# Optimization experiments

Measured on AMD Instinct MI355X. Metric: run time of the kernel, lower is better.

Reference implementation:

```python
import jax, jax.numpy as jnp
import numpy as np


def setup_inputs() -> dict:
    key = jax.random.key(0)
    k1, k2, k3, k4 = jax.random.split(key, 4)
    E = 1_600_000
    N = 100_000
    IN, OUT = 128, 256
    edge_index = jax.random.randint(k1, (2, E), 0, N, dtype=jnp.int32)
    time_encoding = jax.random.normal(k2, (E, IN), dtype=jnp.float32)
    # Linear(in_channels, out_channels): weight [OUT, IN], bias [OUT]
    bound = 1.0 / np.sqrt(IN)
    W = jax.random.uniform(k3, (OUT, IN), minval=-bound, maxval=bound, dtype=jnp.float32)
    b = jax.random.uniform(k4, (OUT,), minval=-bound, maxval=bound, dtype=jnp.float32)
    return {"edge_index": edge_index, "time_encoding": time_encoding,
            "num_nodes": N, "W": W, "b": b}


def reference(edge_index, time_encoding, num_nodes, W, b):
    # scatter-add per-edge time encodings into destination-node buckets
    col = edge_index[1]
    agg = jax.ops.segment_sum(time_encoding, col, num_segments=num_nodes)  # [N, IN]
    # dense projection: Linear -> x @ W.T + b
    return agg @ W.T + b  # [N, OUT]
```

## Files before the change

kernel.cpp:

```cpp
#include <hip/hip_runtime.h>
#include <hip/hip_bf16.h>

#define IN_CH 128
#define OUT_CH 256
#define BLK_SCAN 1024
#define AGG_STRIDE 132

typedef __bf16 bf16x8 __attribute__((ext_vector_type(8)));
typedef float f32x4 __attribute__((ext_vector_type(4)));

__device__ inline unsigned short f2bf(float f) {
  union { float f; unsigned int u; } v; v.f = f;
  unsigned int u = v.u;
  u += 0x7FFFu + ((u >> 16) & 1u);
  return (unsigned short)(u >> 16);
}

__device__ inline float bfhi2f(unsigned int u) {
  union { unsigned int u; float f; } v; v.u = u & 0xFFFF0000u; return v.f;
}
__device__ inline float bflo2f(unsigned int u) {
  union { unsigned int u; float f; } v; v.u = u << 16; return v.f;
}

__global__ void initB_kernel(const float* __restrict__ W, unsigned short* __restrict__ Bpack,
                             int* __restrict__ cnt, int nzero) {
  int i = blockIdx.x * blockDim.x + threadIdx.x;
  if (i < nzero) cnt[i] = 0;
  if (i < IN_CH * OUT_CH) {
    const int j  = i & 7;
    const int c  = (i >> 3) & 15;
    const int kb = (i >> 7) & 3;
    const int ks = (i >> 9) & 3;
    const int tn = i >> 11;
    Bpack[i] = f2bf(W[(size_t)(tn * 16 + c) * IN_CH + ks * 32 + kb * 8 + j]);
  }
}

__global__ void hist_kernel(const int* __restrict__ col, int E, int* __restrict__ count) {
  int i = blockIdx.x * blockDim.x + threadIdx.x;
  int b = i * 4;
  if (b + 4 <= E) {
    const int4 c = *(const int4*)(col + b);
    atomicAdd(&count[c.x], 1);
    atomicAdd(&count[c.y], 1);
    atomicAdd(&count[c.z], 1);
    atomicAdd(&count[c.w], 1);
  } else {
    for (int j = b; j < E; ++j) atomicAdd(&count[col[j]], 1);
  }
}

__global__ __launch_bounds__(BLK_SCAN) void scan_block_kernel(
    const int* __restrict__ count, int N, int* __restrict__ excl, int* __restrict__ bsum) {
  __shared__ int wsum[16];
  const int tid = threadIdx.x;
  const int i = blockIdx.x * BLK_SCAN + tid;
  const int v = (i < N) ? count[i] : 0;
  int x = v;
#pragma unroll
  for (int d = 1; d < 64; d <<= 1) {
    int t = __shfl_up(x, d, 64);
    if ((tid & 63) >= d) x += t;
  }
  if ((tid & 63) == 63) wsum[tid >> 6] = x;
  __syncthreads();
  if (tid < 16) {
    int s = wsum[tid];
#pragma unroll
    for (int d = 1; d < 16; d <<= 1) {
      int t = __shfl_up(s, d, 16);
      if (tid >= d) s += t;
    }
    wsum[tid] = s;
  }
  __syncthreads();
  const int w = tid >> 6;
  const int prefix = (w == 0) ? 0 : wsum[w - 1];
  if (i < N) excl[i] = prefix + x - v;
  if (tid == BLK_SCAN - 1) bsum[blockIdx.x] = prefix + x;
}

__global__ void scan_bsum_kernel(int* __restrict__ bsum, int nb) {
  __shared__ int tmp[256];
  const int tid = threadIdx.x;
  int run = 0;
  for (int s = 0; s < nb; s += 256) {
    int v = (s + tid < nb) ? bsum[s + tid] : 0;
    tmp[tid] = v;
    __syncthreads();
    for (int d = 1; d < 256; d <<= 1) {
      int t = (tid >= d) ? tmp[tid - d] : 0;
      __syncthreads();
      tmp[tid] += t;
      __syncthreads();
    }
    if (s + tid < nb) bsum[s + tid] = run + tmp[tid] - v;
    run += tmp[255];
    __syncthreads();
  }
}

__global__ void add_offsets_kernel(int* __restrict__ excl, const int* __restrict__ bsum,
                                   int* __restrict__ cursor, int N) {
  int i = blockIdx.x * blockDim.x + threadIdx.x;
  if (i < N) {
    int o = excl[i] + bsum[i / BLK_SCAN];
    excl[i] = o;
    cursor[i] = o;
  }
}

__global__ __launch_bounds__(256) void bin_kernel(
    const float* __restrict__ te, const int* __restrict__ col,
    int* __restrict__ cursor, unsigned int* __restrict__ binned, int E) {
  const int lane = threadIdx.x & 63;
  const int gw = (blockIdx.x * 256 + threadIdx.x) >> 6;
  const int nw = (gridDim.x * 256) >> 6;
  for (int base = gw * 8; base < E; base += nw * 8) {
    int ne = E - base; if (ne > 8) ne = 8;
    int mypos = 0;
    if (lane < ne) {
      mypos = atomicAdd(&cursor[col[base + lane]], 1);
    }
#pragma unroll
    for (int j = 0; j < 8; ++j) {
      if (j < ne) {
        const int pos = __builtin_amdgcn_readlane(mypos, j);
        const float2 v = *(const float2*)(te + (size_t)(base + j) * IN_CH + lane * 2);
        binned[(size_t)pos * 64 + lane] =
            (unsigned int)f2bf(v.x) | ((unsigned int)f2bf(v.y) << 16);
      }
    }
  }
}

__global__ __launch_bounds__(256) void phase2_kernel(
    const unsigned int* __restrict__ binned, const int* __restrict__ start,
    const int* __restrict__ cend, const unsigned short* __restrict__ Bpack,
    const float* __restrict__ bias, float* __restrict__ out, int N) {
  __shared__ float agg[16][AGG_STRIDE];
  const int tid = threadIdx.x;
  const int wave = tid >> 6;
  const int lane = tid & 63;
  const int half = lane >> 5;
  const int li   = lane & 31;
  const int m0 = blockIdx.x * 16;

  int s0[4], e0[4];
  float acc[4][4];
  uint2 v[4][8];
#pragma unroll
  for (int q = 0; q < 4; ++q) {
    const int n = m0 + wave * 4 + q;
    s0[q] = (n < N) ? start[n] : 0;
    e0[q] = (n < N) ? cend[n] : 0;
#pragma unroll
    for (int c = 0; c < 4; ++c) acc[q][c] = 0.f;
  }
#pragma unroll
  for (int q = 0; q < 4; ++q) {
#pragma unroll
    for (int j = 0; j < 8; ++j) {
      int row = s0[q] + 2 * j + half;
      row = (row < e0[q]) ? row : (e0[q] > s0[q] ? e0[q] - 1 : 0);
      v[q][j] = *(const uint2*)(binned + (size_t)row * 64 + li * 2);
    }
  }
#pragma unroll
  for (int q = 0; q < 4; ++q) {
    const int rem = e0[q] - s0[q];
#pragma unroll
    for (int j = 0; j < 8; ++j) {
      const float c = (2 * j + half < rem) ? 1.f : 0.f;
      acc[q][0] = fmaf(c, bflo2f(v[q][j].x), acc[q][0]);
      acc[q][1] = fmaf(c, bfhi2f(v[q][j].x), acc[q][1]);
      acc[q][2] = fmaf(c, bflo2f(v[q][j].y), acc[q][2]);
      acc[q][3] = fmaf(c, bfhi2f(v[q][j].y), acc[q][3]);
    }
    for (int r0 = s0[q] + 16; r0 < e0[q]; r0 += 16) {
      const int rem2 = e0[q] - r0;
      uint2 w[8];
#pragma unroll
      for (int j = 0; j < 8; ++j) {
        int row = r0 + 2 * j + half;
        row = (row < e0[q]) ? row : (e0[q] - 1);
        w[j] = *(const uint2*)(binned + (size_t)row * 64 + li * 2);
      }
#pragma unroll
      for (int j = 0; j < 8; ++j) {
        const float c = (2 * j + half < rem2) ? 1.f : 0.f;
        acc[q][0] = fmaf(c, bflo2f(w[j].x), acc[q][0]);
        acc[q][1] = fmaf(c, bfhi2f(w[j].x), acc[q][1]);
        acc[q][2] = fmaf(c, bflo2f(w[j].y), acc[q][2]);
        acc[q][3] = fmaf(c, bfhi2f(w[j].y), acc[q][3]);
      }
    }
    acc[q][0] += __shfl_down(acc[q][0], 32);
    acc[q][1] += __shfl_down(acc[q][1], 32);
    acc[q][2] += __shfl_down(acc[q][2], 32);
    acc[q][3] += __shfl_down(acc[q][3], 32);
    if (half == 0) {
      *(float4*)(&agg[wave * 4 + q][4 * li]) =
          make_float4(acc[q][0], acc[q][1], acc[q][2], acc[q][3]);
    }
  }
  __syncthreads();

  const int r  = lane & 15;
  const int kb = lane >> 4;

  bf16x8 a[4];
#pragma unroll
  for (int ks = 0; ks < 4; ++ks) {
    bf16x8 t;
#pragma unroll
    for (int j = 0; j < 8; ++j) t[j] = (__bf16)agg[r][ks * 32 + kb * 8 + j];
    a[ks] = t;
  }

  f32x4 accm[4];
#pragma unroll
  for (int ct = 0; ct < 4; ++ct) accm[ct] = (f32x4){0.f, 0.f, 0.f, 0.f};

#pragma unroll
  for (int ct = 0; ct < 4; ++ct) {
    const int tn = wave * 4 + ct;
#pragma unroll
    for (int ks = 0; ks < 4; ++ks) {
      const bf16x8 bb = *(const bf16x8*)(Bpack + (size_t)((((tn * 4 + ks) * 4 + kb) * 16 + r) * 8));
      accm[ct] = __builtin_amdgcn_mfma_f32_16x16x32_bf16(a[ks], bb, accm[ct], 0, 0, 0);
    }
  }

#pragma unroll
  for (int ct = 0; ct < 4; ++ct) {
    const int colo = wave * 64 + ct * 16 + r;
    const float bv = bias[colo];
#pragma unroll
    for (int j = 0; j < 4; ++j) {
      const int m = m0 + kb * 4 + j;
      if (m < N) out[(size_t)m * OUT_CH + colo] = accm[ct][j] + bv;
    }
  }
}

extern "C" void kernel_launch(void* const* d_in, const int* in_sizes, int n_in,
                              void* d_out, int out_size, void* d_ws, size_t ws_size,
                              hipStream_t stream) {
  const int* edge_index = (const int*)d_in[0];
  const float* te       = (const float*)d_in[1];
  const float* W        = (const float*)d_in[3];
  const float* bias     = (const float*)d_in[4];
  float* out            = (float*)d_out;

  const int E = in_sizes[0] / 2;
  const int N = out_size / OUT_CH;
  const int* col = edge_index + E;

  const int Np = (N + 3) & ~3;

  char* p = (char*)d_ws;
  unsigned short* Bpack = (unsigned short*)p;      p += 65536;
  int* cnt    = (int*)p;                           p += (size_t)Np * 4;
  int* start  = (int*)p;                           p += (size_t)Np * 4;
  int* cursor = (int*)p;                           p += (size_t)Np * 4;
  int* bsum   = (int*)p;                           p += 4096 * 4;
  p = (char*)(((uintptr_t)p + 255) & ~(uintptr_t)255);
  unsigned int* binned = (unsigned int*)p;

  const int nb = (N + BLK_SCAN - 1) / BLK_SCAN;
  const int init_n = (N > IN_CH * OUT_CH) ? N : IN_CH * OUT_CH;
  const int K = (N + 15) / 16;

  hipLaunchKernelGGL(initB_kernel, dim3((init_n + 255) / 256), dim3(256), 0, stream,
                     W, Bpack, cnt, N);
  hipLaunchKernelGGL(hist_kernel, dim3((E / 4 + 255) / 256), dim3(256), 0, stream,
                     col, E, cnt);
  hipLaunchKernelGGL(scan_block_kernel, dim3(nb), dim3(BLK_SCAN), 0, stream,
                     cnt, N, start, bsum);
  hipLaunchKernelGGL(scan_bsum_kernel, dim3(1), dim3(256), 0, stream, bsum, nb);
  hipLaunchKernelGGL(add_offsets_kernel, dim3((N + 255) / 256), dim3(256), 0, stream,
                     start, bsum, cursor, N);
  hipLaunchKernelGGL(bin_kernel, dim3(2048), dim3(256), 0, stream,
                     te, col, cursor, binned, E);
  hipLaunchKernelGGL(phase2_kernel, dim3(K), dim3(256), 0, stream,
                     binned, start, cursor, Bpack, bias, out, N);
}
```

Before: 453.6 us.

## Split edge binning and aggregation into two chunks with bf16 partial sums

Edges are split into two halves. Each half gets its own histogram and cursor range. The first half is binned and aggregated into a bf16 per-node partial buffer. The second half is then binned and aggregated, and adds the partials before the MFMA projection. The intent is to shrink the binned data in flight between the bin and aggregate passes so more of it stays in the last-level cache instead of going out to HBM. The te loads and output stores also become nontemporal. The cost is two extra kernel launches, an extra write and read of the per-node partial buffer, and an extra bf16 rounding of the partial sums.

```diff
diff --git a/kernel.cpp b/kernel.cpp
--- a/kernel.cpp
+++ b/kernel.cpp
@@ -8,6 +8,7 @@
 
 typedef __bf16 bf16x8 __attribute__((ext_vector_type(8)));
 typedef float f32x4 __attribute__((ext_vector_type(4)));
+typedef float f32x2 __attribute__((ext_vector_type(2)));
 
 __device__ inline unsigned short f2bf(float f) {
   union { float f; unsigned int u; } v; v.f = f;
@@ -15,7 +16,6 @@
   u += 0x7FFFu + ((u >> 16) & 1u);
   return (unsigned short)(u >> 16);
 }
-
 __device__ inline float bfhi2f(unsigned int u) {
   union { unsigned int u; float f; } v; v.u = u & 0xFFFF0000u; return v.f;
 }
@@ -37,26 +37,27 @@
   }
 }
 
-__global__ void hist_kernel(const int* __restrict__ col, int E, int* __restrict__ count) {
+__global__ void hist2_kernel(const int* __restrict__ col, int E, int E2,
+                             int* __restrict__ cnt2, int N) {
   int i = blockIdx.x * blockDim.x + threadIdx.x;
   int b = i * 4;
   if (b + 4 <= E) {
     const int4 c = *(const int4*)(col + b);
-    atomicAdd(&count[c.x], 1);
-    atomicAdd(&count[c.y], 1);
-    atomicAdd(&count[c.z], 1);
-    atomicAdd(&count[c.w], 1);
+    atomicAdd(&cnt2[((b + 0) >= E2 ? N : 0) + c.x], 1);
+    atomicAdd(&cnt2[((b + 1) >= E2 ? N : 0) + c.y], 1);
+    atomicAdd(&cnt2[((b + 2) >= E2 ? N : 0) + c.z], 1);
+    atomicAdd(&cnt2[((b + 3) >= E2 ? N : 0) + c.w], 1);
   } else {
-    for (int j = b; j < E; ++j) atomicAdd(&count[col[j]], 1);
+    for (int j = b; j < E; ++j) atomicAdd(&cnt2[(j >= E2 ? N : 0) + col[j]], 1);
   }
 }
 
 __global__ __launch_bounds__(BLK_SCAN) void scan_block_kernel(
-    const int* __restrict__ count, int N, int* __restrict__ excl, int* __restrict__ bsum) {
+    const int* __restrict__ count, int NN, int* __restrict__ excl, int* __restrict__ bsum) {
   __shared__ int wsum[16];
   const int tid = threadIdx.x;
   const int i = blockIdx.x * BLK_SCAN + tid;
-  const int v = (i < N) ? count[i] : 0;
+  const int v = (i < NN) ? count[i] : 0;
   int x = v;
 #pragma unroll
   for (int d = 1; d < 64; d <<= 1) {
@@ -77,7 +78,7 @@
   __syncthreads();
   const int w = tid >> 6;
   const int prefix = (w == 0) ? 0 : wsum[w - 1];
-  if (i < N) excl[i] = prefix + x - v;
+  if (i < NN) excl[i] = prefix + x - v;
   if (tid == BLK_SCAN - 1) bsum[blockIdx.x] = prefix + x;
 }
 
@@ -102,9 +103,9 @@
 }
 
 __global__ void add_offsets_kernel(int* __restrict__ excl, const int* __restrict__ bsum,
-                                   int* __restrict__ cursor, int N) {
+                                   int* __restrict__ cursor, int NN) {
   int i = blockIdx.x * blockDim.x + threadIdx.x;
-  if (i < N) {
+  if (i < NN) {
     int o = excl[i] + bsum[i / BLK_SCAN];
     excl[i] = o;
     cursor[i] = o;
@@ -113,12 +114,12 @@
 
 __global__ __launch_bounds__(256) void bin_kernel(
     const float* __restrict__ te, const int* __restrict__ col,
-    int* __restrict__ cursor, unsigned int* __restrict__ binned, int E) {
+    int* __restrict__ cursor, unsigned int* __restrict__ binned, int lo, int hi) {
   const int lane = threadIdx.x & 63;
   const int gw = (blockIdx.x * 256 + threadIdx.x) >> 6;
   const int nw = (gridDim.x * 256) >> 6;
-  for (int base = gw * 8; base < E; base += nw * 8) {
-    int ne = E - base; if (ne > 8) ne = 8;
+  for (int base = lo + gw * 8; base < hi; base += nw * 8) {
+    int ne = hi - base; if (ne > 8) ne = 8;
     int mypos = 0;
     if (lane < ne) {
       mypos = atomicAdd(&cursor[col[base + lane]], 1);
@@ -127,18 +128,21 @@
     for (int j = 0; j < 8; ++j) {
       if (j < ne) {
         const int pos = __builtin_amdgcn_readlane(mypos, j);
-        const float2 v = *(const float2*)(te + (size_t)(base + j) * IN_CH + lane * 2);
+        const f32x2 v = __builtin_nontemporal_load(
+            (const f32x2*)(te + (size_t)(base + j) * IN_CH + lane * 2));
         binned[(size_t)pos * 64 + lane] =
-            (unsigned int)f2bf(v.x) | ((unsigned int)f2bf(v.y) << 16);
+            (unsigned int)f2bf(v[0]) | ((unsigned int)f2bf(v[1]) << 16);
       }
     }
   }
 }
 
+template <bool FINAL, bool RAGG>
 __global__ __launch_bounds__(256) void phase2_kernel(
     const unsigned int* __restrict__ binned, const int* __restrict__ start,
-    const int* __restrict__ cend, const unsigned short* __restrict__ Bpack,
-    const float* __restrict__ bias, float* __restrict__ out, int N) {
+    const int* __restrict__ cend, unsigned int* __restrict__ aggrow,
+    const unsigned short* __restrict__ Bpack, const float* __restrict__ bias,
+    float* __restrict__ out, int N) {
   __shared__ float agg[16][AGG_STRIDE];
   const int tid = threadIdx.x;
   const int wave = tid >> 6;
@@ -169,6 +173,7 @@
   }
 #pragma unroll
   for (int q = 0; q < 4; ++q) {
+    const int n = m0 + wave * 4 + q;
     const int rem = e0[q] - s0[q];
 #pragma unroll
     for (int j = 0; j < 8; ++j) {
@@ -196,15 +201,32 @@
         acc[q][3] = fmaf(c, bfhi2f(w[j].y), acc[q][3]);
       }
     }
+    if (RAGG) {
+      const int nn = (n < N) ? n : (N > 0 ? N - 1 : 0);
+      const uint2 va = *(const uint2*)(aggrow + (size_t)nn * 64 + li * 2);
+      const float c = (half == 0 && n < N) ? 1.f : 0.f;
+      acc[q][0] = fmaf(c, bflo2f(va.x), acc[q][0]);
+      acc[q][1] = fmaf(c, bfhi2f(va.x), acc[q][1]);
+      acc[q][2] = fmaf(c, bflo2f(va.y), acc[q][2]);
+      acc[q][3] = fmaf(c, bfhi2f(va.y), acc[q][3]);
+    }
     acc[q][0] += __shfl_down(acc[q][0], 32);
     acc[q][1] += __shfl_down(acc[q][1], 32);
     acc[q][2] += __shfl_down(acc[q][2], 32);
     acc[q][3] += __shfl_down(acc[q][3], 32);
     if (half == 0) {
-      *(float4*)(&agg[wave * 4 + q][4 * li]) =
-          make_float4(acc[q][0], acc[q][1], acc[q][2], acc[q][3]);
-    }
-  }
+      if (FINAL) {
+        *(float4*)(&agg[wave * 4 + q][4 * li]) =
+            make_float4(acc[q][0], acc[q][1], acc[q][2], acc[q][3]);
+      } else if (n < N) {
+        uint2 o;
+        o.x = (unsigned int)f2bf(acc[q][0]) | ((unsigned int)f2bf(acc[q][1]) << 16);
+        o.y = (unsigned int)f2bf(acc[q][2]) | ((unsigned int)f2bf(acc[q][3]) << 16);
+        *(uint2*)(aggrow + (size_t)n * 64 + li * 2) = o;
+      }
+    }
+  }
+  if (!FINAL) return;
   __syncthreads();
 
   const int r  = lane & 15;
@@ -240,7 +262,7 @@
 #pragma unroll
     for (int j = 0; j < 4; ++j) {
       const int m = m0 + kb * 4 + j;
-      if (m < N) out[(size_t)m * OUT_CH + colo] = accm[ct][j] + bv;
+      if (m < N) __builtin_nontemporal_store(accm[ct][j] + bv, &out[(size_t)m * OUT_CH + colo]);
     }
   }
 }
@@ -258,32 +280,47 @@
   const int N = out_size / OUT_CH;
   const int* col = edge_index + E;
 
-  const int Np = (N + 3) & ~3;
+  const int NN = 2 * N;
 
   char* p = (char*)d_ws;
   unsigned short* Bpack = (unsigned short*)p;      p += 65536;
-  int* cnt    = (int*)p;                           p += (size_t)Np * 4;
-  int* start  = (int*)p;                           p += (size_t)Np * 4;
-  int* cursor = (int*)p;                           p += (size_t)Np * 4;
+  int* cnt2   = (int*)p;                           p += (size_t)NN * 4;
+  int* cursor = (int*)p;                           p += (size_t)NN * 4;
   int* bsum   = (int*)p;                           p += 4096 * 4;
   p = (char*)(((uintptr_t)p + 255) & ~(uintptr_t)255);
-  unsigned int* binned = (unsigned int*)p;
-
-  const int nb = (N + BLK_SCAN - 1) / BLK_SCAN;
-  const int init_n = (N > IN_CH * OUT_CH) ? N : IN_CH * OUT_CH;
+  unsigned int* aggrow = (unsigned int*)p;         p += (size_t)N * 256;
+  unsigned int* binned = (unsigned int*)p;         p += (size_t)E * 256;
+  const size_t need2 = (size_t)(p - (char*)d_ws);
+
+  const bool two_chunk = (ws_size >= need2);
+  if (!two_chunk) binned = aggrow;
+
+  const int E2 = two_chunk ? (E / 2) : E;
+  const int nb = (NN + BLK_SCAN - 1) / BLK_SCAN;
+  const int init_n = (NN > IN_CH * OUT_CH) ? NN : IN_CH * OUT_CH;
   const int K = (N + 15) / 16;
 
   hipLaunchKernelGGL(initB_kernel, dim3((init_n + 255) / 256), dim3(256), 0, stream,
-                     W, Bpack, cnt, N);
-  hipLaunchKernelGGL(hist_kernel, dim3((E / 4 + 255) / 256), dim3(256), 0, stream,
-                     col, E, cnt);
+                     W, Bpack, cnt2, NN);
+  hipLaunchKernelGGL(hist2_kernel, dim3((E / 4 + 255) / 256), dim3(256), 0, stream,
+                     col, E, E2, cnt2, N);
   hipLaunchKernelGGL(scan_block_kernel, dim3(nb), dim3(BLK_SCAN), 0, stream,
-                     cnt, N, start, bsum);
+                     cnt2, NN, cnt2, bsum);
   hipLaunchKernelGGL(scan_bsum_kernel, dim3(1), dim3(256), 0, stream, bsum, nb);
-  hipLaunchKernelGGL(add_offsets_kernel, dim3((N + 255) / 256), dim3(256), 0, stream,
-                     start, bsum, cursor, N);
+  hipLaunchKernelGGL(add_offsets_kernel, dim3((NN + 255) / 256), dim3(256), 0, stream,
+                     cnt2, bsum, cursor, NN);
+
   hipLaunchKernelGGL(bin_kernel, dim3(2048), dim3(256), 0, stream,
-                     te, col, cursor, binned, E);
-  hipLaunchKernelGGL(phase2_kernel, dim3(K), dim3(256), 0, stream,
-                     binned, start, cursor, Bpack, bias, out, N);
-}
+                     te, col, cursor, binned, 0, E2);
+  if (two_chunk) {
+    hipLaunchKernelGGL((phase2_kernel<false, false>), dim3(K), dim3(256), 0, stream,
+                       binned, cnt2, cursor, aggrow, Bpack, bias, out, N);
+    hipLaunchKernelGGL(bin_kernel, dim3(2048), dim3(256), 0, stream,
+                       te, col, cursor + N, binned, E2, E);
+    hipLaunchKernelGGL((phase2_kernel<true, true>), dim3(K), dim3(256), 0, stream,
+                       binned, cnt2 + N, cursor + N, aggrow, Bpack, bias, out, N);
+  } else {
+    hipLaunchKernelGGL((phase2_kernel<true, false>), dim3(K), dim3(256), 0, stream,
+                       binned, cnt2, cursor, aggrow, Bpack, bias, out, N);
+  }
+}
```

Measured after the change: 498.3 us. 9.8% more time.
